# Kernel optimization log

Measured on AMD Instinct MI355X. Metric: run time of the kernel, lower is better.

The kernel has to match this reference:

```python
import jax, jax.numpy as jnp
import numpy as np

VOCAB, HID, LSTM_H, T_LEN, N_LAB, BATCH = 21128, 768, 128, 256, 9, 32


def _gru_dir(x, Wih, Whh, bih, bhh):
    # x: [B,T,D]; PyTorch GRU gate order: reset, update, new
    xp = jnp.einsum('btd,gd->tbg', x, Wih) + bih  # [T,B,3H]
    H = Whh.shape[1]
    def step(h, xt):
        gh = h @ Whh.T + bhh
        xr, xz, xn = jnp.split(xt, 3, axis=-1)
        hr, hz, hn = jnp.split(gh, 3, axis=-1)
        r = jax.nn.sigmoid(xr + hr)
        z = jax.nn.sigmoid(xz + hz)
        n = jnp.tanh(xn + r * hn)
        hnew = (1.0 - z) * n + z * h
        return hnew, hnew
    h0 = jnp.zeros((x.shape[0], H), x.dtype)
    _, hs = jax.lax.scan(step, h0, xp)
    return hs  # [T,B,H]


def _crf_llh(emissions, labels, trans, start, end):
    # emissions [B,T,L], labels [B,T]; full mask (all ones)
    e = jnp.transpose(emissions, (1, 0, 2))  # [T,B,L]
    emit_scores = jnp.take_along_axis(e, labels.T[:, :, None], axis=2)[:, :, 0]  # [T,B]
    trans_scores = trans[labels[:, :-1], labels[:, 1:]]  # [B,T-1]
    num = start[labels[:, 0]] + emit_scores.sum(0) + trans_scores.sum(1) + end[labels[:, -1]]
    def step(alpha, et):
        alpha = jax.nn.logsumexp(alpha[:, :, None] + trans[None] + et[:, None, :], axis=1)
        return alpha, None
    alpha0 = start + e[0]
    alpha, _ = jax.lax.scan(step, alpha0, e[1:])
    denom = jax.nn.logsumexp(alpha + end, axis=1)
    return num - denom  # [B]


def _viterbi(emissions, trans, start, end):
    e = jnp.transpose(emissions, (1, 0, 2))  # [T,B,L]
    def step(alpha, et):
        scores = alpha[:, :, None] + trans[None]  # [B,L_prev,L_cur]
        bp = jnp.argmax(scores, axis=1)
        alpha = jnp.max(scores, axis=1) + et
        return alpha, bp
    alpha0 = start + e[0]
    alpha, bps = jax.lax.scan(step, alpha0, e[1:])  # bps: [T-1,B,L]
    last = jnp.argmax(alpha + end, axis=1)  # [B]
    def back(y, bp):
        yprev = jnp.take_along_axis(bp, y[:, None], axis=1)[:, 0]
        return yprev, yprev
    _, path = jax.lax.scan(back, last, bps, reverse=True)  # [T-1,B]
    return jnp.concatenate([path, last[None]], axis=0).T  # [B,T]


def setup_inputs() -> dict:
    key = jax.random.key(0)
    ks = jax.random.split(key, 16)
    s = 0.02
    inp = {
        'input_ids': jax.random.randint(ks[0], (BATCH, T_LEN), 0, VOCAB),
        'attention_mask': jnp.ones((BATCH, T_LEN), jnp.int64 if jax.config.jax_enable_x64 else jnp.int32),
        'labels': jax.random.randint(ks[1], (BATCH, T_LEN), 0, N_LAB),
        'emb': jax.random.normal(ks[2], (VOCAB, HID), jnp.float32) * s,
        'Wih_f': jax.random.normal(ks[3], (3 * LSTM_H, HID), jnp.float32) * s,
        'Whh_f': jax.random.normal(ks[4], (3 * LSTM_H, LSTM_H), jnp.float32) * s,
        'bih_f': jnp.zeros((3 * LSTM_H,), jnp.float32),
        'bhh_f': jnp.zeros((3 * LSTM_H,), jnp.float32),
        'Wih_b': jax.random.normal(ks[5], (3 * LSTM_H, HID), jnp.float32) * s,
        'Whh_b': jax.random.normal(ks[6], (3 * LSTM_H, LSTM_H), jnp.float32) * s,
        'bih_b': jnp.zeros((3 * LSTM_H,), jnp.float32),
        'bhh_b': jnp.zeros((3 * LSTM_H,), jnp.float32),
        'Wlin': jax.random.normal(ks[7], (N_LAB, 2 * LSTM_H), jnp.float32) * s,
        'blin': jnp.zeros((N_LAB,), jnp.float32),
        'trans': jax.random.normal(ks[8], (N_LAB, N_LAB), jnp.float32) * 0.1,
        'start': jax.random.normal(ks[9], (N_LAB,), jnp.float32) * 0.1,
        'end': jax.random.normal(ks[10], (N_LAB,), jnp.float32) * 0.1,
    }
    return inp


def reference(input_ids, attention_mask, labels, emb, Wih_f, Whh_f, bih_f, bhh_f,
              Wih_b, Whh_b, bih_b, bhh_b, Wlin, blin, trans, start, end):
    x = emb[input_ids]  # [B,T,HID]
    hf = _gru_dir(x, Wih_f, Whh_f, bih_f, bhh_f)                 # [T,B,H]
    hb = _gru_dir(x[:, ::-1, :], Wih_b, Whh_b, bih_b, bhh_b)[::-1]  # [T,B,H]
    seq = jnp.concatenate([hf, hb], axis=-1).transpose(1, 0, 2)  # [B,T,2H]
    emissions = seq @ Wlin.T + blin                              # [B,T,L]
    decoded = _viterbi(emissions, trans, start, end)             # [B,T] int
    llh = _crf_llh(emissions, labels, trans, start, end)         # [B]
    loss = -jnp.mean(llh)
    return decoded, loss
```

## Files before the change

### kernel.cpp

```cpp
#include <hip/hip_runtime.h>
#include <math.h>

#define T_LEN 256
#define BATCH 32
#define HID   768
#define GH    384
#define LH    128
#define NLAB  9
#define M_TOT (T_LEN*BATCH)

typedef float v2f __attribute__((ext_vector_type(2)));
typedef _Float16 h8 __attribute__((ext_vector_type(8)));
typedef float f4 __attribute__((ext_vector_type(4)));

#define LO_SCALE 1024.f
#define LO_INV   (1.f/1024.f)

#define BC(x, i) __int_as_float(__builtin_amdgcn_ds_swizzle(__float_as_int(x), (i) << 5))

#define DPP_ADD(x, ctrl) \
  ((x) + __int_as_float(__builtin_amdgcn_update_dpp(0, __float_as_int(x), (ctrl), 0xF, 0xF, true)))

#define BAR_LGKM() do {                                   \
    asm volatile("s_waitcnt lgkmcnt(0)" ::: "memory");    \
    __builtin_amdgcn_s_barrier();                         \
    asm volatile("" ::: "memory");                        \
  } while (0)

__global__ __launch_bounds__(256, 2) void k_gemm_xp(
    const int* __restrict__ ids, const float* __restrict__ emb,
    const float* __restrict__ Wf, const float* __restrict__ Wb,
    const float* __restrict__ bihf, const float* __restrict__ bihb,
    float* __restrict__ xp)
{
  __shared__ __align__(16) _Float16 Ah[128*40];
  __shared__ __align__(16) _Float16 Al[128*40];
  __shared__ __align__(16) _Float16 Bh[128*40];
  __shared__ __align__(16) _Float16 Bl[128*40];

  const int tid  = threadIdx.x;
  const int lane = tid & 63, w = tid >> 6;
  const int m0 = blockIdx.y * 128, n0 = blockIdx.x * 128;

  const int srow = tid >> 1, sk = (tid & 1) * 16;
  const int gm = m0 + srow;
  const int tok = ids[(gm & 31) * T_LEN + (gm >> 5)];
  const float* aG = emb + (size_t)tok * HID + sk;
  const int gn = n0 + srow;
  const float* bG = (gn < GH ? Wf + (size_t)gn * HID
                             : Wb + (size_t)(gn - GH) * HID) + sk;

  const int fr = lane & 15, fq = lane >> 4;
  const int mrow = (w & 1) * 64;
  const int ncol = (w >> 1) * 64;

  f4 acc[4][4];
  f4 acc2[4][4];
#pragma unroll
  for (int i = 0; i < 4; ++i)
#pragma unroll
    for (int j = 0; j < 4; ++j) { acc[i][j] = f4{0,0,0,0}; acc2[i][j] = f4{0,0,0,0}; }

  const int sb = srow * 40 + sk;

  float4 ra[4], rb[4];
#pragma unroll
  for (int c = 0; c < 4; ++c) {
    ra[c] = *reinterpret_cast<const float4*>(aG + 4 * c);
    rb[c] = *reinterpret_cast<const float4*>(bG + 4 * c);
  }

  for (int kt = 0; kt < HID / 32; ++kt) {
    __syncthreads();
#pragma unroll
    for (int m = 0; m < 2; ++m) {
      const float4* src = m ? rb : ra;
      _Float16* dsth = m ? Bh : Ah;
      _Float16* dstl = m ? Bl : Al;
#pragma unroll
      for (int seg = 0; seg < 2; ++seg) {
        float xs[8] = {src[2*seg].x, src[2*seg].y, src[2*seg].z, src[2*seg].w,
                       src[2*seg+1].x, src[2*seg+1].y, src[2*seg+1].z, src[2*seg+1].w};
        h8 hi, lo;
#pragma unroll
        for (int c = 0; c < 8; ++c) {
          _Float16 h = (_Float16)xs[c];
          hi[c] = h;
          lo[c] = (_Float16)((xs[c] - (float)h) * LO_SCALE);
        }
        *reinterpret_cast<h8*>(&dsth[sb + seg * 8]) = hi;
        *reinterpret_cast<h8*>(&dstl[sb + seg * 8]) = lo;
      }
    }
    if (kt + 1 < HID / 32) {
      const float* pa = aG + (kt + 1) * 32;
      const float* pb = bG + (kt + 1) * 32;
#pragma unroll
      for (int c = 0; c < 4; ++c) {
        ra[c] = *reinterpret_cast<const float4*>(pa + 4 * c);
        rb[c] = *reinterpret_cast<const float4*>(pb + 4 * c);
      }
    }
    __syncthreads();

    h8 fbh[4], fbl[4];
#pragma unroll
    for (int j = 0; j < 4; ++j) {
      const int off = (ncol + j * 16 + fr) * 40 + fq * 8;
      fbh[j] = *reinterpret_cast<const h8*>(&Bh[off]);
      fbl[j] = *reinterpret_cast<const h8*>(&Bl[off]);
    }
#pragma unroll
    for (int i = 0; i < 4; ++i) {
      const int off = (mrow + i * 16 + fr) * 40 + fq * 8;
      h8 fah = *reinterpret_cast<const h8*>(&Ah[off]);
      h8 fal = *reinterpret_cast<const h8*>(&Al[off]);
#pragma unroll
      for (int j = 0; j < 4; ++j) {
        acc[i][j]  = __builtin_amdgcn_mfma_f32_16x16x32_f16(fah, fbh[j], acc[i][j],  0, 0, 0);
        acc2[i][j] = __builtin_amdgcn_mfma_f32_16x16x32_f16(fah, fbl[j], acc2[i][j], 0, 0, 0);
        acc2[i][j] = __builtin_amdgcn_mfma_f32_16x16x32_f16(fal, fbh[j], acc2[i][j], 0, 0, 0);
      }
    }
  }

  float bcol[4];
#pragma unroll
  for (int j = 0; j < 4; ++j) {
    const int c = n0 + ncol + j * 16 + fr;
    bcol[j] = (c < GH) ? bihf[c] : bihb[c - GH];
  }
#pragma unroll
  for (int i = 0; i < 4; ++i)
#pragma unroll
    for (int j = 0; j < 4; ++j) {
      const int col = n0 + ncol + j * 16 + fr;
#pragma unroll
      for (int r = 0; r < 4; ++r) {
        const int row = m0 + mrow + i * 16 + fq * 4 + r;
        xp[(size_t)row * HID + col] = acc[i][j][r] + acc2[i][j][r] * LO_INV + bcol[j];
      }
    }
}

__global__ __attribute__((amdgpu_flat_work_group_size(512, 512),
                          amdgpu_waves_per_eu(2, 2)))
void k_gru(
    const float* __restrict__ xp,
    const float* __restrict__ Whhf, const float* __restrict__ Whhb,
    const float* __restrict__ bhhf, const float* __restrict__ bhhb,
    float* __restrict__ hbuf, float* __restrict__ lossp)
{
  __shared__ __align__(16) float hsp[2][144];
  const int tid = threadIdx.x;
  const int g   = tid >> 2;
  const int q   = tid & 3;
  const int bd  = blockIdx.x;
  const int dir = bd >> 5, b = bd & 31;
  const float* Whh = dir ? Whhb : Whhf;
  const float* bhh = dir ? bhhb : bhhf;

  if (bd == 0 && tid == 0) *lossp = 0.f;

  v2f w[3][16];
#pragma unroll
  for (int gate = 0; gate < 3; ++gate) {
    const float* wrow = Whh + (size_t)(gate * LH + g) * LH + q * 32;
#pragma unroll
    for (int j = 0; j < 8; ++j) {
      float4 w4 = *reinterpret_cast<const float4*>(wrow + j * 4);
      w[gate][2*j]   = v2f{w4.x, w4.y};
      w[gate][2*j+1] = v2f{w4.z, w4.w};
    }
  }
  const float br = bhh[g], bz = bhh[g + LH], bn = bhh[g + 2*LH];

  if (tid < LH) hsp[0][36*(tid >> 5) + (tid & 31)] = 0.f;

  const int t0   = dir ? (T_LEN - 1) : 0;
  const int dt   = dir ? -1 : 1;
  const float* xbase = xp + (size_t)b * HID + dir * GH + g;
  float* hob = hbuf + (size_t)b * 256 + dir * LH + g;

  float xr = 0.f, xz = 0.f, xn = 0.f;
  if (q == 0) {
    const float* p = xbase + (size_t)t0 * BATCH * HID;
    xr = p[0]; xz = p[LH]; xn = p[2*LH];
  }
  float hprev = 0.f;
  BAR_LGKM();

  int t = t0;
  for (int step = 0; step < T_LEN; ++step) {
    const int tn = (step < T_LEN - 1) ? (t + dt) : t;
    float xrn = 0.f, xzn = 0.f, xnn = 0.f;
    if (q == 0) {
      const float* p = xbase + (size_t)tn * BATCH * HID;
      xrn = p[0]; xzn = p[LH]; xnn = p[2*LH];
    }

    const float* hc = &hsp[step & 1][36 * q];
    v2f ar0 = v2f{0.f,0.f}, ar1 = ar0, az0 = ar0, az1 = ar0, an0 = ar0, an1 = ar0;
#pragma unroll
    for (int j = 0; j < 4; ++j) {
      float4 ha = *reinterpret_cast<const float4*>(hc + 8*j);
      float4 hb = *reinterpret_cast<const float4*>(hc + 8*j + 4);
      v2f h0 = v2f{ha.x, ha.y}, h1 = v2f{ha.z, ha.w};
      v2f h2 = v2f{hb.x, hb.y}, h3 = v2f{hb.z, hb.w};
      ar0 = __builtin_elementwise_fma(w[0][4*j+0], h0, ar0);
      ar1 = __builtin_elementwise_fma(w[0][4*j+1], h1, ar1);
      ar0 = __builtin_elementwise_fma(w[0][4*j+2], h2, ar0);
      ar1 = __builtin_elementwise_fma(w[0][4*j+3], h3, ar1);
      az0 = __builtin_elementwise_fma(w[1][4*j+0], h0, az0);
      az1 = __builtin_elementwise_fma(w[1][4*j+1], h1, az1);
      az0 = __builtin_elementwise_fma(w[1][4*j+2], h2, az0);
      az1 = __builtin_elementwise_fma(w[1][4*j+3], h3, az1);
      an0 = __builtin_elementwise_fma(w[2][4*j+0], h0, an0);
      an1 = __builtin_elementwise_fma(w[2][4*j+1], h1, an1);
      an0 = __builtin_elementwise_fma(w[2][4*j+2], h2, an0);
      an1 = __builtin_elementwise_fma(w[2][4*j+3], h3, an1);
    }
    float ar = (ar0.x + ar0.y) + (ar1.x + ar1.y);
    float az = (az0.x + az0.y) + (az1.x + az1.y);
    float an = (an0.x + an0.y) + (an1.x + an1.y);
    ar = DPP_ADD(ar, 0xB1); ar = DPP_ADD(ar, 0x4E);
    az = DPP_ADD(az, 0xB1); az = DPP_ADD(az, 0x4E);
    an = DPP_ADD(an, 0xB1); an = DPP_ADD(an, 0x4E);

    if (q == 0) {
      float r  = __builtin_amdgcn_rcpf(1.f + __expf(-(xr + ar + br)));
      float z  = __builtin_amdgcn_rcpf(1.f + __expf(-(xz + az + bz)));
      float e2 = __expf(2.f * (xn + r * (an + bn)));
      float n  = (e2 - 1.f) * __builtin_amdgcn_rcpf(e2 + 1.f);
      float hnew = (1.f - z) * n + z * hprev;
      hprev = hnew;
      hsp[(step + 1) & 1][36*(g >> 5) + (g & 31)] = hnew;
      hob[(size_t)t * BATCH * 256] = hnew;
    }
    BAR_LGKM();
    xr = xrn; xz = xzn; xn = xnn;
    t = tn;
  }
}

__global__ __launch_bounds__(256, 1) void k_crf_fused(
    const float* __restrict__ hbuf, const float* __restrict__ Wlin,
    const float* __restrict__ blin, const int* __restrict__ labels,
    const float* __restrict__ trans, const float* __restrict__ start,
    const float* __restrict__ endv, float* __restrict__ dec_out,
    float* __restrict__ lossp)
{
  __shared__ float el[T_LEN * 10];
  __shared__ __align__(16) unsigned char bp8[(T_LEN - 1) * 16];
  const int b    = blockIdx.x;
  const int tid  = threadIdx.x;
  const int lane = tid & 63, w = tid >> 6;
  const int sub  = lane >> 4, l16 = lane & 15;

  float4 wreg[NLAB][4];
#pragma unroll
  for (int j = 0; j < NLAB; ++j)
#pragma unroll
    for (int c = 0; c < 4; ++c)
      wreg[j][c] = *reinterpret_cast<const float4*>(Wlin + j * 256 + l16 * 16 + c * 4);

  for (int k = 0; k < 16; ++k) {
    const int t = w * 64 + k * 4 + sub;
    const float* hp = hbuf + ((size_t)t * BATCH + b) * 256 + l16 * 16;
    const float4 h0 = *reinterpret_cast<const float4*>(hp);
    const float4 h1 = *reinterpret_cast<const float4*>(hp + 4);
    const float4 h2 = *reinterpret_cast<const float4*>(hp + 8);
    const float4 h3 = *reinterpret_cast<const float4*>(hp + 12);
    float acc[NLAB];
#pragma unroll
    for (int j = 0; j < NLAB; ++j) {
      const float4 w0 = wreg[j][0], w1 = wreg[j][1], w2 = wreg[j][2], w3 = wreg[j][3];
      float s0 = h0.x*w0.x + h0.y*w0.y + h0.z*w0.z + h0.w*w0.w;
      float s1 = h1.x*w1.x + h1.y*w1.y + h1.z*w1.z + h1.w*w1.w;
      float s2 = h2.x*w2.x + h2.y*w2.y + h2.z*w2.z + h2.w*w2.w;
      float s3 = h3.x*w3.x + h3.y*w3.y + h3.z*w3.z + h3.w*w3.w;
      acc[j] = (s0 + s1) + (s2 + s3);
    }
#pragma unroll
    for (int j = 0; j < NLAB; ++j) {
#pragma unroll
      for (int off = 1; off < 16; off <<= 1)
        acc[j] += __shfl_xor(acc[j], off);
    }
    if (l16 < NLAB) {
      float v = acc[0];
#pragma unroll
      for (int j = 1; j < NLAB; ++j) v = (l16 == j) ? acc[j] : v;
      el[t * 10 + l16] = v + blin[l16];
    }
  }
  __syncthreads();

  if (w == 0) {
    float tcol[NLAB];
#pragma unroll
    for (int i = 0; i < NLAB; ++i)
      tcol[i] = (lane < NLAB) ? trans[i * NLAB + lane] : 0.f;
    float alpha = (lane < NLAB) ? (start[lane] + el[lane]) : -3e38f;
    float et_next = (lane < NLAB) ? el[10 + lane] : 0.f;
    for (int s = 0; s < T_LEN - 1; ++s) {
      const float et = et_next;
      if (s < T_LEN - 2)
        et_next = (lane < NLAB) ? el[(s + 2) * 10 + lane] : 0.f;
      float v[NLAB];
      v[0] = BC(alpha, 0) + tcol[0];
      v[1] = BC(alpha, 1) + tcol[1];
      v[2] = BC(alpha, 2) + tcol[2];
      v[3] = BC(alpha, 3) + tcol[3];
      v[4] = BC(alpha, 4) + tcol[4];
      v[5] = BC(alpha, 5) + tcol[5];
      v[6] = BC(alpha, 6) + tcol[6];
      v[7] = BC(alpha, 7) + tcol[7];
      v[8] = BC(alpha, 8) + tcol[8];
      float v01 = (v[0] >= v[1]) ? v[0] : v[1];  int i01 = (v[0] >= v[1]) ? 0 : 1;
      float v23 = (v[2] >= v[3]) ? v[2] : v[3];  int i23 = (v[2] >= v[3]) ? 2 : 3;
      float v45 = (v[4] >= v[5]) ? v[4] : v[5];  int i45 = (v[4] >= v[5]) ? 4 : 5;
      float v67 = (v[6] >= v[7]) ? v[6] : v[7];  int i67 = (v[6] >= v[7]) ? 6 : 7;
      float va = (v01 >= v23) ? v01 : v23;       int ia = (v01 >= v23) ? i01 : i23;
      float vb = (v45 >= v67) ? v45 : v67;       int ib = (v45 >= v67) ? i45 : i67;
      float vc = (va >= vb) ? va : vb;           int ic = (va >= vb) ? ia : ib;
      float best = (vc >= v[8]) ? vc : v[8];     int bi = (vc >= v[8]) ? ic : 8;
      alpha = best + et;
      if (lane < NLAB) bp8[s * 16 + lane] = (unsigned char)bi;
    }
    float fin = alpha + ((lane < NLAB) ? endv[lane] : 0.f);
    float fv[NLAB];
    fv[0] = BC(fin, 0); fv[1] = BC(fin, 1); fv[2] = BC(fin, 2);
    fv[3] = BC(fin, 3); fv[4] = BC(fin, 4); fv[5] = BC(fin, 5);
    fv[6] = BC(fin, 6); fv[7] = BC(fin, 7); fv[8] = BC(fin, 8);
    float f01 = (fv[0] >= fv[1]) ? fv[0] : fv[1];  int j01 = (fv[0] >= fv[1]) ? 0 : 1;
    float f23 = (fv[2] >= fv[3]) ? fv[2] : fv[3];  int j23 = (fv[2] >= fv[3]) ? 2 : 3;
    float f45 = (fv[4] >= fv[5]) ? fv[4] : fv[5];  int j45 = (fv[4] >= fv[5]) ? 4 : 5;
    float f67 = (fv[6] >= fv[7]) ? fv[6] : fv[7];  int j67 = (fv[6] >= fv[7]) ? 6 : 7;
    float fa = (f01 >= f23) ? f01 : f23;           int ja = (f01 >= f23) ? j01 : j23;
    float fb = (f45 >= f67) ? f45 : f67;           int jb = (f45 >= f67) ? j45 : j67;
    float fc = (fa >= fb) ? fa : fb;               int jc = (fa >= fb) ? ja : jb;
    int last = (fc >= fv[8]) ? jc : 8;
    if (lane == 0) {
      int y = last;
      dec_out[b * T_LEN + (T_LEN - 1)] = (float)y;
      uint4 row = *reinterpret_cast<const uint4*>(&bp8[(T_LEN - 2) * 16]);
      for (int s = T_LEN - 2; s >= 0; --s) {
        uint4 nrow = row;
        if (s > 0) nrow = *reinterpret_cast<const uint4*>(&bp8[(s - 1) * 16]);
        unsigned wsel = (y < 4) ? row.x : ((y < 8) ? row.y : row.z);
        y = (int)((wsel >> ((y & 3) * 8)) & 0xffu);
        dec_out[b * T_LEN + s] = (float)y;
        row = nrow;
      }
    }
  } else if (w == 1) {
    float tcol[NLAB];
#pragma unroll
    for (int i = 0; i < NLAB; ++i)
      tcol[i] = (lane < NLAB) ? trans[i * NLAB + lane] : 0.f;
    float ca = (lane < NLAB) ? (start[lane] + el[lane]) : -3e38f;
    float et_next = (lane < NLAB) ? el[10 + lane] : 0.f;
    for (int s = 0; s < T_LEN - 1; ++s) {
      const float et = et_next;
      if (s < T_LEN - 2)
        et_next = (lane < NLAB) ? el[(s + 2) * 10 + lane] : 0.f;
      float c[NLAB];
      c[0] = BC(ca, 0) + tcol[0];
      c[1] = BC(ca, 1) + tcol[1];
      c[2] = BC(ca, 2) + tcol[2];
      c[3] = BC(ca, 3) + tcol[3];
      c[4] = BC(ca, 4) + tcol[4];
      c[5] = BC(ca, 5) + tcol[5];
      c[6] = BC(ca, 6) + tcol[6];
      c[7] = BC(ca, 7) + tcol[7];
      c[8] = BC(ca, 8) + tcol[8];
      float m01 = fmaxf(c[0], c[1]), m23 = fmaxf(c[2], c[3]);
      float m45 = fmaxf(c[4], c[5]), m67 = fmaxf(c[6], c[7]);
      float m = fmaxf(fmaxf(fmaxf(m01, m23), fmaxf(m45, m67)), c[8]);
      float p0 = __expf(c[0]-m) + __expf(c[1]-m), p1 = __expf(c[2]-m) + __expf(c[3]-m);
      float p2 = __expf(c[4]-m) + __expf(c[5]-m), p3 = __expf(c[6]-m) + __expf(c[7]-m);
      float p = ((p0 + p1) + (p2 + p3)) + __expf(c[8]-m);
      ca = m + __logf(p) + et;
    }
    float fv[NLAB];
    fv[0] = BC(ca, 0) + endv[0];
    fv[1] = BC(ca, 1) + endv[1];
    fv[2] = BC(ca, 2) + endv[2];
    fv[3] = BC(ca, 3) + endv[3];
    fv[4] = BC(ca, 4) + endv[4];
    fv[5] = BC(ca, 5) + endv[5];
    fv[6] = BC(ca, 6) + endv[6];
    fv[7] = BC(ca, 7) + endv[7];
    fv[8] = BC(ca, 8) + endv[8];
    float mx = -3e38f;
#pragma unroll
    for (int j = 0; j < NLAB; ++j) mx = fmaxf(mx, fv[j]);
    float ps = 0.f;
#pragma unroll
    for (int j = 0; j < NLAB; ++j) ps += __expf(fv[j] - mx);
    float denom = mx + __logf(ps);

    const int* lb = labels + b * T_LEN;
    float part = 0.f;
    for (int t4 = 0; t4 < 4; ++t4) {
      int t = lane * 4 + t4;
      int l = lb[t];
      part += el[t * 10 + l];
      if (t > 0) part += trans[lb[t - 1] * NLAB + l];
    }
#pragma unroll
    for (int off = 32; off > 0; off >>= 1) part += __shfl_xor(part, off);
    if (lane == 0) {
      float num = part + start[lb[0]] + endv[lb[T_LEN - 1]];
      float llh = num - denom;
      atomicAdd(lossp, -llh * (1.0f / BATCH));
    }
  }
}

extern "C" void kernel_launch(void* const* d_in, const int* in_sizes, int n_in,
                              void* d_out, int out_size, void* d_ws, size_t ws_size,
                              hipStream_t stream) {
  const int*   ids    = (const int*)d_in[0];
  const int*   labels = (const int*)d_in[2];
  const float* emb    = (const float*)d_in[3];
  const float* Wihf   = (const float*)d_in[4];
  const float* Whhf   = (const float*)d_in[5];
  const float* bihf   = (const float*)d_in[6];
  const float* bhhf   = (const float*)d_in[7];
  const float* Wihb   = (const float*)d_in[8];
  const float* Whhb   = (const float*)d_in[9];
  const float* bihb   = (const float*)d_in[10];
  const float* bhhb   = (const float*)d_in[11];
  const float* Wlin   = (const float*)d_in[12];
  const float* blin   = (const float*)d_in[13];
  const float* trans  = (const float*)d_in[14];
  const float* start  = (const float*)d_in[15];
  const float* endv   = (const float*)d_in[16];

  float* xp    = (float*)d_ws;
  float* hbuf  = xp + (size_t)M_TOT * HID;
  float* out   = (float*)d_out;
  float* lossp = out + M_TOT;

  k_gemm_xp<<<dim3(6, 64), 256, 0, stream>>>(ids, emb, Wihf, Wihb, bihf, bihb, xp);
  k_gru<<<64, 512, 0, stream>>>(xp, Whhf, Whhb, bhhf, bhhb, hbuf, lossp);
  k_crf_fused<<<BATCH, 256, 0, stream>>>(hbuf, Wlin, blin, labels, trans,
                                         start, endv, out, lossp);
}
```

Baseline: 387.7 us.

## Rewrite GRU recurrence loop as hand-scheduled inline assembly

The GRU recurrent step is replaced with a hand-written GCN assembly loop that pins weights in fixed VGPRs, prefetches the next timestep's input projections, uses ds_swizzle for the cross-lane reduction, and ping-pongs the hidden-state LDS buffer by XORing addresses. The goal is to shorten the per-step serial latency chain (LDS read, FMA, reduce, activation, barrier) that dominates the 256-step recurrence. The GEMM kernel's __syncthreads calls are also replaced with an explicit lgkmcnt wait plus s_barrier. In exchange the inline asm is fragile: it hard-codes register numbers, does not wait on vmcnt before the final store, and depends on manually placed s_nop hazard padding.

```diff
diff --git a/kernel.cpp b/kernel.cpp
--- a/kernel.cpp
+++ b/kernel.cpp
@@ -17,9 +17,6 @@
 #define LO_INV   (1.f/1024.f)
 
 #define BC(x, i) __int_as_float(__builtin_amdgcn_ds_swizzle(__float_as_int(x), (i) << 5))
-
-#define DPP_ADD(x, ctrl) \
-  ((x) + __int_as_float(__builtin_amdgcn_update_dpp(0, __float_as_int(x), (ctrl), 0xF, 0xF, true)))
 
 #define BAR_LGKM() do {                                   \
     asm volatile("s_waitcnt lgkmcnt(0)" ::: "memory");    \
@@ -71,7 +68,7 @@
   }
 
   for (int kt = 0; kt < HID / 32; ++kt) {
-    __syncthreads();
+    BAR_LGKM();
 #pragma unroll
     for (int m = 0; m < 2; ++m) {
       const float4* src = m ? rb : ra;
@@ -101,7 +98,7 @@
         rb[c] = *reinterpret_cast<const float4*>(pb + 4 * c);
       }
     }
-    __syncthreads();
+    BAR_LGKM();
 
     h8 fbh[4], fbl[4];
 #pragma unroll
@@ -151,7 +148,7 @@
     const float* __restrict__ bhhf, const float* __restrict__ bhhb,
     float* __restrict__ hbuf, float* __restrict__ lossp)
 {
-  __shared__ __align__(16) float hsp[2][144];
+  __shared__ __align__(1024) float hsp[2][256];
   const int tid = threadIdx.x;
   const int g   = tid >> 2;
   const int q   = tid & 3;
@@ -162,85 +159,222 @@
 
   if (bd == 0 && tid == 0) *lossp = 0.f;
 
-  v2f w[3][16];
-#pragma unroll
-  for (int gate = 0; gate < 3; ++gate) {
-    const float* wrow = Whh + (size_t)(gate * LH + g) * LH + q * 32;
-#pragma unroll
-    for (int j = 0; j < 8; ++j) {
-      float4 w4 = *reinterpret_cast<const float4*>(wrow + j * 4);
-      w[gate][2*j]   = v2f{w4.x, w4.y};
-      w[gate][2*j+1] = v2f{w4.z, w4.w};
-    }
-  }
   const float br = bhh[g], bz = bhh[g + LH], bn = bhh[g + 2*LH];
-
-  if (tid < LH) hsp[0][36*(tid >> 5) + (tid & 31)] = 0.f;
-
-  const int t0   = dir ? (T_LEN - 1) : 0;
-  const int dt   = dir ? -1 : 1;
-  const float* xbase = xp + (size_t)b * HID + dir * GH + g;
-  float* hob = hbuf + (size_t)b * 256 + dir * LH + g;
-
-  float xr = 0.f, xz = 0.f, xn = 0.f;
-  if (q == 0) {
-    const float* p = xbase + (size_t)t0 * BATCH * HID;
-    xr = p[0]; xz = p[LH]; xn = p[2*LH];
-  }
-  float hprev = 0.f;
+  const float* wg0 = Whh + (size_t)(0*LH + g) * LH + q * 32;
+  const float* wg1 = Whh + (size_t)(1*LH + g) * LH + q * 32;
+  const float* wg2 = Whh + (size_t)(2*LH + g) * LH + q * 32;
+
+  const int t0 = dir ? (T_LEN - 1) : 0;
+  const int dt = dir ? -1 : 1;
+  const float* px = xp + (size_t)t0 * BATCH * HID + b * HID + dir * GH + g;
+  float*       ph = hbuf + (size_t)t0 * BATCH * 256 + b * 256 + dir * LH + g;
+
+  const long long xs = (long long)dt * BATCH * HID * 4;
+  const long long hs = (long long)dt * BATCH * 256 * 4;
+  const unsigned xslo = (unsigned)(xs & 0xffffffffll);
+  const int      xshi = (int)(xs >> 32);
+  const unsigned hslo = (unsigned)(hs & 0xffffffffll);
+  const int      hshi = (int)(hs >> 32);
+  const unsigned xlo = (unsigned)(uintptr_t)px, xhi = (unsigned)((uintptr_t)px >> 32);
+  const unsigned hlo = (unsigned)(uintptr_t)ph, hhi = (unsigned)((uintptr_t)ph >> 32);
+  const unsigned rd0 = (unsigned)(uintptr_t)(&hsp[0][36 * q]);
+  const unsigned wr0 = (unsigned)(uintptr_t)(&hsp[1][36 * (g >> 5) + (g & 31)]);
+
+  if (tid < LH) hsp[0][36 * (tid >> 5) + (tid & 31)] = 0.f;
   BAR_LGKM();
 
-  int t = t0;
-  for (int step = 0; step < T_LEN; ++step) {
-    const int tn = (step < T_LEN - 1) ? (t + dt) : t;
-    float xrn = 0.f, xzn = 0.f, xnn = 0.f;
-    if (q == 0) {
-      const float* p = xbase + (size_t)tn * BATCH * HID;
-      xrn = p[0]; xzn = p[LH]; xnn = p[2*LH];
-    }
-
-    const float* hc = &hsp[step & 1][36 * q];
-    v2f ar0 = v2f{0.f,0.f}, ar1 = ar0, az0 = ar0, az1 = ar0, an0 = ar0, an1 = ar0;
-#pragma unroll
-    for (int j = 0; j < 4; ++j) {
-      float4 ha = *reinterpret_cast<const float4*>(hc + 8*j);
-      float4 hb = *reinterpret_cast<const float4*>(hc + 8*j + 4);
-      v2f h0 = v2f{ha.x, ha.y}, h1 = v2f{ha.z, ha.w};
-      v2f h2 = v2f{hb.x, hb.y}, h3 = v2f{hb.z, hb.w};
-      ar0 = __builtin_elementwise_fma(w[0][4*j+0], h0, ar0);
-      ar1 = __builtin_elementwise_fma(w[0][4*j+1], h1, ar1);
-      ar0 = __builtin_elementwise_fma(w[0][4*j+2], h2, ar0);
-      ar1 = __builtin_elementwise_fma(w[0][4*j+3], h3, ar1);
-      az0 = __builtin_elementwise_fma(w[1][4*j+0], h0, az0);
-      az1 = __builtin_elementwise_fma(w[1][4*j+1], h1, az1);
-      az0 = __builtin_elementwise_fma(w[1][4*j+2], h2, az0);
-      az1 = __builtin_elementwise_fma(w[1][4*j+3], h3, az1);
-      an0 = __builtin_elementwise_fma(w[2][4*j+0], h0, an0);
-      an1 = __builtin_elementwise_fma(w[2][4*j+1], h1, an1);
-      an0 = __builtin_elementwise_fma(w[2][4*j+2], h2, an0);
-      an1 = __builtin_elementwise_fma(w[2][4*j+3], h3, an1);
-    }
-    float ar = (ar0.x + ar0.y) + (ar1.x + ar1.y);
-    float az = (az0.x + az0.y) + (az1.x + az1.y);
-    float an = (an0.x + an0.y) + (an1.x + an1.y);
-    ar = DPP_ADD(ar, 0xB1); ar = DPP_ADD(ar, 0x4E);
-    az = DPP_ADD(az, 0xB1); az = DPP_ADD(az, 0x4E);
-    an = DPP_ADD(an, 0xB1); an = DPP_ADD(an, 0x4E);
-
-    if (q == 0) {
-      float r  = __builtin_amdgcn_rcpf(1.f + __expf(-(xr + ar + br)));
-      float z  = __builtin_amdgcn_rcpf(1.f + __expf(-(xz + az + bz)));
-      float e2 = __expf(2.f * (xn + r * (an + bn)));
-      float n  = (e2 - 1.f) * __builtin_amdgcn_rcpf(e2 + 1.f);
-      float hnew = (1.f - z) * n + z * hprev;
-      hprev = hnew;
-      hsp[(step + 1) & 1][36*(g >> 5) + (g & 31)] = hnew;
-      hob[(size_t)t * BATCH * 256] = hnew;
-    }
-    BAR_LGKM();
-    xr = xrn; xz = xzn; xn = xnn;
-    t = tn;
-  }
+  int cnt = T_LEN;
+  asm volatile(
+    "global_load_dwordx4 v[128:131], %[wg0], off\n\t"
+    "global_load_dwordx4 v[132:135], %[wg0], off offset:16\n\t"
+    "global_load_dwordx4 v[136:139], %[wg0], off offset:32\n\t"
+    "global_load_dwordx4 v[140:143], %[wg0], off offset:48\n\t"
+    "global_load_dwordx4 v[144:147], %[wg0], off offset:64\n\t"
+    "global_load_dwordx4 v[148:151], %[wg0], off offset:80\n\t"
+    "global_load_dwordx4 v[152:155], %[wg0], off offset:96\n\t"
+    "global_load_dwordx4 v[156:159], %[wg0], off offset:112\n\t"
+    "global_load_dwordx4 v[160:163], %[wg1], off\n\t"
+    "global_load_dwordx4 v[164:167], %[wg1], off offset:16\n\t"
+    "global_load_dwordx4 v[168:171], %[wg1], off offset:32\n\t"
+    "global_load_dwordx4 v[172:175], %[wg1], off offset:48\n\t"
+    "global_load_dwordx4 v[176:179], %[wg1], off offset:64\n\t"
+    "global_load_dwordx4 v[180:183], %[wg1], off offset:80\n\t"
+    "global_load_dwordx4 v[184:187], %[wg1], off offset:96\n\t"
+    "global_load_dwordx4 v[188:191], %[wg1], off offset:112\n\t"
+    "global_load_dwordx4 v[192:195], %[wg2], off\n\t"
+    "global_load_dwordx4 v[196:199], %[wg2], off offset:16\n\t"
+    "global_load_dwordx4 v[200:203], %[wg2], off offset:32\n\t"
+    "global_load_dwordx4 v[204:207], %[wg2], off offset:48\n\t"
+    "global_load_dwordx4 v[208:211], %[wg2], off offset:64\n\t"
+    "global_load_dwordx4 v[212:215], %[wg2], off offset:80\n\t"
+    "global_load_dwordx4 v[216:219], %[wg2], off offset:96\n\t"
+    "global_load_dwordx4 v[220:223], %[wg2], off offset:112\n\t"
+    "v_mov_b32 v96, %[xlo]\n\t"
+    "v_mov_b32 v97, %[xhi]\n\t"
+    "v_mov_b32 v98, %[hlo]\n\t"
+    "v_mov_b32 v99, %[hhi]\n\t"
+    "v_mov_b32 v100, %[rd0]\n\t"
+    "v_mov_b32 v101, %[wr0]\n\t"
+    "global_load_dword v107, v[96:97], off\n\t"
+    "global_load_dword v108, v[96:97], off offset:512\n\t"
+    "global_load_dword v109, v[96:97], off offset:1024\n\t"
+    "v_mov_b32 v110, 0\n\t"
+    "s_waitcnt vmcnt(0)\n\t"
+    "0:\n\t"
+    "s_waitcnt vmcnt(1)\n\t"
+    "v_mov_b32 v104, v107\n\t"
+    "v_mov_b32 v105, v108\n\t"
+    "v_mov_b32 v106, v109\n\t"
+    "ds_read_b128 v[224:227], v100\n\t"
+    "ds_read_b128 v[228:231], v100 offset:16\n\t"
+    "ds_read_b128 v[232:235], v100 offset:32\n\t"
+    "ds_read_b128 v[236:239], v100 offset:48\n\t"
+    "ds_read_b128 v[240:243], v100 offset:64\n\t"
+    "ds_read_b128 v[244:247], v100 offset:80\n\t"
+    "ds_read_b128 v[248:251], v100 offset:96\n\t"
+    "ds_read_b128 v[252:255], v100 offset:112\n\t"
+    "s_cmp_lg_u32 %[cnt], 1\n\t"
+    "s_cbranch_scc0 2f\n\t"
+    "v_add_co_u32 v96, vcc, %[xslo], v96\n\t"
+    "v_addc_co_u32 v97, vcc, %[xshi], v97, vcc\n\t"
+    "global_load_dword v107, v[96:97], off\n\t"
+    "global_load_dword v108, v[96:97], off offset:512\n\t"
+    "global_load_dword v109, v[96:97], off offset:1024\n\t"
+    "2:\n\t"
+    "s_waitcnt lgkmcnt(0)\n\t"
+    "v_pk_mul_f32 v[116:117], v[128:129], v[224:225]\n\t"
+    "v_pk_mul_f32 v[118:119], v[130:131], v[226:227]\n\t"
+    "v_pk_fma_f32 v[116:117], v[132:133], v[228:229], v[116:117]\n\t"
+    "v_pk_fma_f32 v[118:119], v[134:135], v[230:231], v[118:119]\n\t"
+    "v_pk_fma_f32 v[116:117], v[136:137], v[232:233], v[116:117]\n\t"
+    "v_pk_fma_f32 v[118:119], v[138:139], v[234:235], v[118:119]\n\t"
+    "v_pk_fma_f32 v[116:117], v[140:141], v[236:237], v[116:117]\n\t"
+    "v_pk_fma_f32 v[118:119], v[142:143], v[238:239], v[118:119]\n\t"
+    "v_pk_fma_f32 v[116:117], v[144:145], v[240:241], v[116:117]\n\t"
+    "v_pk_fma_f32 v[118:119], v[146:147], v[242:243], v[118:119]\n\t"
+    "v_pk_fma_f32 v[116:117], v[148:149], v[244:245], v[116:117]\n\t"
+    "v_pk_fma_f32 v[118:119], v[150:151], v[246:247], v[118:119]\n\t"
+    "v_pk_fma_f32 v[116:117], v[152:153], v[248:249], v[116:117]\n\t"
+    "v_pk_fma_f32 v[118:119], v[154:155], v[250:251], v[118:119]\n\t"
+    "v_pk_fma_f32 v[116:117], v[156:157], v[252:253], v[116:117]\n\t"
+    "v_pk_fma_f32 v[118:119], v[158:159], v[254:255], v[118:119]\n\t"
+    "v_pk_mul_f32 v[120:121], v[160:161], v[224:225]\n\t"
+    "v_pk_mul_f32 v[122:123], v[162:163], v[226:227]\n\t"
+    "v_pk_fma_f32 v[120:121], v[164:165], v[228:229], v[120:121]\n\t"
+    "v_pk_fma_f32 v[122:123], v[166:167], v[230:231], v[122:123]\n\t"
+    "v_pk_fma_f32 v[120:121], v[168:169], v[232:233], v[120:121]\n\t"
+    "v_pk_fma_f32 v[122:123], v[170:171], v[234:235], v[122:123]\n\t"
+    "v_pk_fma_f32 v[120:121], v[172:173], v[236:237], v[120:121]\n\t"
+    "v_pk_fma_f32 v[122:123], v[174:175], v[238:239], v[122:123]\n\t"
+    "v_pk_fma_f32 v[120:121], v[176:177], v[240:241], v[120:121]\n\t"
+    "v_pk_fma_f32 v[122:123], v[178:179], v[242:243], v[122:123]\n\t"
+    "v_pk_fma_f32 v[120:121], v[180:181], v[244:245], v[120:121]\n\t"
+    "v_pk_fma_f32 v[122:123], v[182:183], v[246:247], v[122:123]\n\t"
+    "v_pk_fma_f32 v[120:121], v[184:185], v[248:249], v[120:121]\n\t"
+    "v_pk_fma_f32 v[122:123], v[186:187], v[250:251], v[122:123]\n\t"
+    "v_pk_fma_f32 v[120:121], v[188:189], v[252:253], v[120:121]\n\t"
+    "v_pk_fma_f32 v[122:123], v[190:191], v[254:255], v[122:123]\n\t"
+    "v_pk_mul_f32 v[124:125], v[192:193], v[224:225]\n\t"
+    "v_pk_mul_f32 v[126:127], v[194:195], v[226:227]\n\t"
+    "v_pk_fma_f32 v[124:125], v[196:197], v[228:229], v[124:125]\n\t"
+    "v_pk_fma_f32 v[126:127], v[198:199], v[230:231], v[126:127]\n\t"
+    "v_pk_fma_f32 v[124:125], v[200:201], v[232:233], v[124:125]\n\t"
+    "v_pk_fma_f32 v[126:127], v[202:203], v[234:235], v[126:127]\n\t"
+    "v_pk_fma_f32 v[124:125], v[204:205], v[236:237], v[124:125]\n\t"
+    "v_pk_fma_f32 v[126:127], v[206:207], v[238:239], v[126:127]\n\t"
+    "v_pk_fma_f32 v[124:125], v[208:209], v[240:241], v[124:125]\n\t"
+    "v_pk_fma_f32 v[126:127], v[210:211], v[242:243], v[126:127]\n\t"
+    "v_pk_fma_f32 v[124:125], v[212:213], v[244:245], v[124:125]\n\t"
+    "v_pk_fma_f32 v[126:127], v[214:215], v[246:247], v[126:127]\n\t"
+    "v_pk_fma_f32 v[124:125], v[216:217], v[248:249], v[124:125]\n\t"
+    "v_pk_fma_f32 v[126:127], v[218:219], v[250:251], v[126:127]\n\t"
+    "v_pk_fma_f32 v[124:125], v[220:221], v[252:253], v[124:125]\n\t"
+    "v_pk_fma_f32 v[126:127], v[222:223], v[254:255], v[126:127]\n\t"
+    "v_add_f32 v116, v116, v117\n\t"
+    "v_add_f32 v118, v118, v119\n\t"
+    "v_add_f32 v116, v116, v118\n\t"
+    "v_add_f32 v120, v120, v121\n\t"
+    "v_add_f32 v122, v122, v123\n\t"
+    "v_add_f32 v120, v120, v122\n\t"
+    "v_add_f32 v124, v124, v125\n\t"
+    "v_add_f32 v126, v126, v127\n\t"
+    "v_add_f32 v124, v124, v126\n\t"
+    "ds_swizzle_b32 v111, v116 offset:0x041F\n\t"
+    "ds_swizzle_b32 v112, v120 offset:0x041F\n\t"
+    "ds_swizzle_b32 v113, v124 offset:0x041F\n\t"
+    "s_waitcnt lgkmcnt(0)\n\t"
+    "v_add_f32 v116, v116, v111\n\t"
+    "v_add_f32 v120, v120, v112\n\t"
+    "v_add_f32 v124, v124, v113\n\t"
+    "ds_swizzle_b32 v111, v116 offset:0x081F\n\t"
+    "ds_swizzle_b32 v112, v120 offset:0x081F\n\t"
+    "ds_swizzle_b32 v113, v124 offset:0x081F\n\t"
+    "s_waitcnt lgkmcnt(0)\n\t"
+    "v_add_f32 v116, v116, v111\n\t"
+    "v_add_f32 v120, v120, v112\n\t"
+    "v_add_f32 v124, v124, v113\n\t"
+    "v_add_f32 v111, v104, v116\n\t"
+    "v_add_f32 v112, v105, v120\n\t"
+    "v_add_f32 v113, v124, %[bn]\n\t"
+    "v_add_f32 v111, v111, %[br]\n\t"
+    "v_add_f32 v112, v112, %[bz]\n\t"
+    "v_mul_f32 v111, 0xbfb8aa3b, v111\n\t"
+    "v_mul_f32 v112, 0xbfb8aa3b, v112\n\t"
+    "v_exp_f32 v111, v111\n\t"
+    "v_exp_f32 v112, v112\n\t"
+    "s_nop 0\n\t"
+    "v_add_f32 v111, 1.0, v111\n\t"
+    "v_add_f32 v112, 1.0, v112\n\t"
+    "v_rcp_f32 v111, v111\n\t"
+    "v_rcp_f32 v112, v112\n\t"
+    "s_nop 0\n\t"
+    "v_fmac_f32 v106, v111, v113\n\t"
+    "v_mul_f32 v113, 0x4038aa3b, v106\n\t"
+    "v_exp_f32 v113, v113\n\t"
+    "v_sub_f32 v115, 1.0, v112\n\t"
+    "s_nop 0\n\t"
+    "v_add_f32 v114, -1.0, v113\n\t"
+    "v_add_f32 v113, 1.0, v113\n\t"
+    "v_rcp_f32 v113, v113\n\t"
+    "s_nop 1\n\t"
+    "v_mul_f32 v114, v114, v113\n\t"
+    "v_mul_f32 v115, v115, v114\n\t"
+    "v_fmac_f32 v115, v112, v110\n\t"
+    "v_mov_b32 v110, v115\n\t"
+    "ds_write_b32 v101, v115\n\t"
+    "global_store_dword v[98:99], v115, off\n\t"
+    "v_add_co_u32 v98, vcc, %[hslo], v98\n\t"
+    "v_addc_co_u32 v99, vcc, %[hshi], v99, vcc\n\t"
+    "v_xor_b32 v100, 0x400, v100\n\t"
+    "v_xor_b32 v101, 0x400, v101\n\t"
+    "s_waitcnt lgkmcnt(0)\n\t"
+    "s_barrier\n\t"
+    "s_sub_u32 %[cnt], %[cnt], 1\n\t"
+    "s_cmp_lg_u32 %[cnt], 0\n\t"
+    "s_cbranch_scc1 0b\n\t"
+    : [cnt]"+s"(cnt)
+    : [wg0]"v"(wg0), [wg1]"v"(wg1), [wg2]"v"(wg2),
+      [xlo]"v"(xlo), [xhi]"v"(xhi), [hlo]"v"(hlo), [hhi]"v"(hhi),
+      [rd0]"v"(rd0), [wr0]"v"(wr0),
+      [br]"v"(br), [bz]"v"(bz), [bn]"v"(bn),
+      [xslo]"s"(xslo), [xshi]"v"(xshi), [hslo]"s"(hslo), [hshi]"v"(hshi)
+    : "memory", "vcc", "scc",
+      "v96","v97","v98","v99","v100","v101","v102","v103","v104","v105",
+      "v106","v107","v108","v109","v110","v111","v112","v113","v114","v115",
+      "v116","v117","v118","v119","v120","v121","v122","v123","v124","v125",
+      "v126","v127","v128","v129","v130","v131","v132","v133","v134","v135",
+      "v136","v137","v138","v139","v140","v141","v142","v143","v144","v145",
+      "v146","v147","v148","v149","v150","v151","v152","v153","v154","v155",
+      "v156","v157","v158","v159","v160","v161","v162","v163","v164","v165",
+      "v166","v167","v168","v169","v170","v171","v172","v173","v174","v175",
+      "v176","v177","v178","v179","v180","v181","v182","v183","v184","v185",
+      "v186","v187","v188","v189","v190","v191","v192","v193","v194","v195",
+      "v196","v197","v198","v199","v200","v201","v202","v203","v204","v205",
+      "v206","v207","v208","v209","v210","v211","v212","v213","v214","v215",
+      "v216","v217","v218","v219","v220","v221","v222","v223","v224","v225",
+      "v226","v227","v228","v229","v230","v231","v232","v233","v234","v235",
+      "v236","v237","v238","v239","v240","v241","v242","v243","v244","v245",
+      "v246","v247","v248","v249","v250","v251","v252","v253","v254","v255");
 }
 
 __global__ __launch_bounds__(256, 1) void k_crf_fused(
```

Result: no change. 393.9 us (+1.6%).
